# Kernel tuning notes

Measured on AMD Instinct MI355X. Metric: run time of the kernel, lower is better.

## Reference

```python
import jax, jax.numpy as jnp
import numpy as np
import math

DIM = 1024
MAX_DEPTH = 16
ROPE_BASE = 10000.0
NUM_ACTIVE = 2

def setup_inputs() -> dict:
    key = jax.random.key(0)
    ks = jax.random.split(key, 6)
    bsz, seq, dim, E, hidden = 4, 1024, DIM, 8, 4 * DIM
    bound = 1.0 / math.sqrt(dim)
    return {
        "x": jax.random.normal(ks[0], (bsz, seq, dim), jnp.float32),
        "router_w": jax.random.normal(ks[1], (dim, dim), jnp.float32) * 0.02,
        "expert_keys": jax.random.uniform(ks[2], (E, dim), jnp.float32, -bound, bound),
        "expert_bias": jnp.zeros((E,), jnp.float32),
        "fc_w": jax.random.normal(ks[3], (E, hidden, dim), jnp.float32) * 0.02,
        "proj_w": jax.random.normal(ks[4], (E, dim, hidden), jnp.float32) * 0.02,
        "depth_idx": 3,
    }

def _rope_row(depth_idx, rev_idx, dtype):
    half = DIM // 2
    inv_freq = 1.0 / (ROPE_BASE ** (jnp.arange(0, DIM, 2, dtype=jnp.float32) / DIM))  # [half]
    f = depth_idx * inv_freq
    r = rev_idx * inv_freq
    return (jnp.cos(f).astype(dtype), jnp.sin(f).astype(dtype),
            jnp.cos(r).astype(dtype), jnp.sin(r).astype(dtype))

def reference(x, router_w, expert_keys, expert_bias, fc_w, proj_w, depth_idx):
    bsz, seq, dim = x.shape
    N = bsz * seq
    flat_x = x.reshape(N, dim)
    # router + RMSNorm (no weight, eps = machine eps, matching F.rms_norm default)
    q = flat_x @ router_w.T
    eps = jnp.asarray(jnp.finfo(q.dtype).eps, q.dtype)
    q = q * jax.lax.rsqrt(jnp.mean(q * q, axis=-1, keepdims=True) + eps)
    # depth RoPE (forward freq on first half pairing, reverse freq on second half)
    half = dim // 2
    cos, sin, rcos, rsin = _rope_row(float(depth_idx), float(MAX_DEPTH - 1 - depth_idx), q.dtype)
    q1, q2 = q[..., :half], q[..., half:]
    q = jnp.concatenate((q1 * cos + q2 * sin, -q1 * rsin + q2 * rcos), axis=-1)
    # routing
    logits = (q @ expert_keys.T) / math.sqrt(dim)  # [N, E]
    gate_values = jax.nn.sigmoid(logits)
    biased = logits + expert_bias
    _, topk_idx = jax.lax.top_k(biased, NUM_ACTIVE)  # [N, k]
    topk_gates = jnp.take_along_axis(gate_values, topk_idx, axis=-1)
    topk_gates = topk_gates / jnp.clip(topk_gates.sum(-1, keepdims=True), 1e-9, None)
    gates = jnp.zeros_like(gate_values).at[jnp.arange(N)[:, None], topk_idx].set(topk_gates)
    # dense all-expert MLP: relu(x W_fc^T)^2 W_proj^T, then mask-and-sum
    h = jax.nn.relu(jnp.einsum('nd,ehd->neh', flat_x, fc_w))
    expert_out = jnp.einsum('neh,edh->ned', h * h, proj_w)  # [N, E, dim]
    y = jnp.einsum('ned,ne->nd', expert_out, gates)
    return y.reshape(bsz, seq, dim)
```

## Files before the change

kernel.cpp:

```cpp
#include <hip/hip_runtime.h>
#include <hip/hip_bf16.h>
#include <math.h>

#define N_TOK 4096
#define DIM_V 1024
#define NEXP  8
#define HID   4096
#define NSLOT 9216

typedef short  s16x8 __attribute__((ext_vector_type(8)));
typedef unsigned short u16x8 __attribute__((ext_vector_type(8)));
typedef float  f32x4 __attribute__((ext_vector_type(4)));

constexpr size_t OFF_XB   = 0;
constexpr size_t OFF_WB   = OFF_XB + 8388608;
constexpr size_t OFF_RK   = OFF_WB + 2097152;
constexpr size_t OFF_KPP  = OFF_RK + 65536;
constexpr size_t OFF_SSQ  = OFF_KPP + 65536;
constexpr size_t OFF_CNT  = OFF_SSQ + 16384;
constexpr size_t OFF_CUR  = OFF_CNT + 128;
constexpr size_t OFF_TOK  = OFF_CUR + 128;
constexpr size_t OFF_GSL  = OFF_TOK + 36864;
constexpr size_t ZERO_BEG = OFF_KPP;
constexpr size_t ZERO_END = OFF_GSL + 36864;
constexpr size_t OFF_OFFP = ZERO_END;
constexpr size_t OFF_IDX2 = OFF_OFFP + 128;
constexpr size_t OFF_G2   = OFF_IDX2 + 32768;
constexpr size_t OFF_INV  = OFF_G2 + 32768;
constexpr size_t SMALL_END = OFF_INV + 32768;

constexpr size_t A_OFF_FCB = SMALL_END;
constexpr size_t A_OFF_PO  = A_OFF_FCB;
constexpr size_t A_OFF_PJB = A_OFF_FCB + 67108864;
constexpr size_t A_OFF_H2  = A_OFF_PJB + 67108864;
constexpr size_t WS_FULL   = A_OFF_H2 + 75497472;

__device__ inline unsigned short f2bf(float f) {
  __hip_bfloat16 h = __float2bfloat16(f);
  return __builtin_bit_cast(unsigned short, h);
}

__device__ __forceinline__ void gload16(const void* g, void* l) {
  __builtin_amdgcn_global_load_lds(
      (const __attribute__((address_space(1))) unsigned int*)g,
      (__attribute__((address_space(3))) unsigned int*)l, 16, 0, 0);
}

__global__ void k_cvt(const float* __restrict__ s, unsigned short* __restrict__ d, int n8) {
  for (int i = blockIdx.x * blockDim.x + threadIdx.x; i < n8;
       i += gridDim.x * blockDim.x) {
    float4 a = ((const float4*)s)[2 * i];
    float4 b = ((const float4*)s)[2 * i + 1];
    u16x8 o = { f2bf(a.x), f2bf(a.y), f2bf(a.z), f2bf(a.w),
                f2bf(b.x), f2bf(b.y), f2bf(b.z), f2bf(b.w) };
    *(u16x8*)(d + (size_t)i * 8) = o;
  }
}

__global__ void k_ropekeys(const float* __restrict__ keys, const int* __restrict__ depth,
                           double* __restrict__ rk) {
  int i = threadIdx.x;
  if (i >= 512) return;
  int dep = depth[0];
  double p = pow(10000.0, (double)i / 512.0);
  float invf = 1.0f / (float)p;
  float ff = (float)dep * invf;
  float rr = (float)(15 - dep) * invf;
  float cf  = (float)cos((double)ff);
  float sf  = (float)sin((double)ff);
  float rcf = (float)cos((double)rr);
  float rsf = (float)sin((double)rr);
  for (int e = 0; e < NEXP; ++e) {
    double k1 = (double)keys[e * DIM_V + i];
    double k2 = (double)keys[e * DIM_V + 512 + i];
    rk[e * DIM_V + i]       = (double)cf  * k1 - (double)rsf * k2;
    rk[e * DIM_V + 512 + i] = (double)sf  * k1 + (double)rcf * k2;
  }
}

__global__ __launch_bounds__(256) void k_colsum(const float* __restrict__ W,
                                                const double* __restrict__ rk,
                                                double* __restrict__ kpp) {
  int j  = blockIdx.x * 256 + threadIdx.x;
  int d0 = blockIdx.y * 64;
  double acc[NEXP] = {};
  for (int dd = 0; dd < 64; ++dd) {
    int d = d0 + dd;
    double w = (double)W[(size_t)d * DIM_V + j];
#pragma unroll
    for (int e = 0; e < NEXP; ++e) acc[e] += w * rk[e * DIM_V + d];
  }
  for (int e = 0; e < NEXP; ++e) atomicAdd(&kpp[e * DIM_V + j], acc[e]);
}

__global__ __launch_bounds__(256) void k_qt(const unsigned short* __restrict__ xb,
                                            const unsigned short* __restrict__ wb,
                                            float* __restrict__ sumsq) {
  __shared__ alignas(16) unsigned short As[128][64];
  __shared__ alignas(16) unsigned short Bs[128][64];
  const int m0 = blockIdx.x * 128, n0 = blockIdx.y * 128;
  const int tid = threadIdx.x, wid = tid >> 6, lane = tid & 63;
  const int wr = (wid >> 1) * 64, wc = (wid & 1) * 64;
  const int srow = tid >> 3, scol = (tid & 7) * 8;
  f32x4 acc[4][4] = {};
  for (int k0 = 0; k0 < DIM_V; k0 += 64) {
    __syncthreads();
#pragma unroll
    for (int p = 0; p < 4; ++p)
      gload16(xb + (size_t)(m0 + p * 32 + srow) * DIM_V + k0 + scol,
              (char*)As + p * 4096 + wid * 1024);
#pragma unroll
    for (int p = 0; p < 4; ++p)
      gload16(wb + (size_t)(n0 + p * 32 + srow) * DIM_V + k0 + scol,
              (char*)Bs + p * 4096 + wid * 1024);
    __syncthreads();
#pragma unroll
    for (int kk = 0; kk < 64; kk += 32) {
      s16x8 af[4], bfv[4];
#pragma unroll
      for (int m = 0; m < 4; ++m)
        af[m] = *(const s16x8*)&As[wr + m * 16 + (lane & 15)][kk + (lane >> 4) * 8];
#pragma unroll
      for (int n = 0; n < 4; ++n)
        bfv[n] = *(const s16x8*)&Bs[wc + n * 16 + (lane & 15)][kk + (lane >> 4) * 8];
#pragma unroll
      for (int m = 0; m < 4; ++m)
#pragma unroll
        for (int n = 0; n < 4; ++n)
          acc[m][n] = __builtin_amdgcn_mfma_f32_16x16x32_bf16(af[m], bfv[n], acc[m][n], 0, 0, 0);
    }
  }
#pragma unroll
  for (int m = 0; m < 4; ++m)
#pragma unroll
    for (int j = 0; j < 4; ++j) {
      float s = 0.f;
#pragma unroll
      for (int n = 0; n < 4; ++n) { float v = acc[m][n][j]; s += v * v; }
      s += __shfl_xor(s, 1, 64); s += __shfl_xor(s, 2, 64);
      s += __shfl_xor(s, 4, 64); s += __shfl_xor(s, 8, 64);
      if ((lane & 15) == 0)
        atomicAdd(&sumsq[m0 + wr + m * 16 + (lane >> 4) * 4 + j], s);
    }
}

__global__ __launch_bounds__(256) void k_gate(const float* __restrict__ x,
                                              const double* __restrict__ kpp,
                                              const float* __restrict__ sumsq,
                                              const float* __restrict__ bias,
                                              int* __restrict__ idx2, float* __restrict__ gates2,
                                              int* __restrict__ counts) {
  int wave = (blockIdx.x * 256 + threadIdx.x) >> 6;
  int lane = threadIdx.x & 63;
  if (wave >= N_TOK) return;
  const float4* xr = (const float4*)(x + (size_t)wave * DIM_V);
  double a[NEXP] = {};
#pragma unroll
  for (int j = 0; j < 4; ++j) {
    int c = lane + 64 * j;
    float4 v = xr[c];
#pragma unroll
    for (int e = 0; e < NEXP; ++e) {
      const double* kp = kpp + (size_t)e * DIM_V + c * 4;
      a[e] += (double)v.x * kp[0] + (double)v.y * kp[1] +
              (double)v.z * kp[2] + (double)v.w * kp[3];
    }
  }
#pragma unroll
  for (int e = 0; e < NEXP; ++e)
    for (int d = 1; d < 64; d <<= 1) a[e] += __shfl_xor(a[e], d, 64);
  if (lane == 0) {
    float s = rsqrtf(sumsq[wave] * (1.0f / 1024.0f) + 1.1920928955078125e-7f);
    float z[NEXP], b[NEXP];
#pragma unroll
    for (int e = 0; e < NEXP; ++e) {
      z[e] = (float)(a[e] * (double)s * (1.0 / 32.0));
      b[e] = z[e] + bias[e];
    }
    int i1 = 0;
    for (int e = 1; e < NEXP; ++e) if (b[e] > b[i1]) i1 = e;
    int i2 = -1;
    for (int e = 0; e < NEXP; ++e) if (e != i1 && (i2 < 0 || b[e] > b[i2])) i2 = e;
    float g1 = 1.f / (1.f + expf(-z[i1]));
    float g2 = 1.f / (1.f + expf(-z[i2]));
    float sm = fmaxf(g1 + g2, 1e-9f);
    idx2[wave * 2] = i1; idx2[wave * 2 + 1] = i2;
    gates2[wave * 2] = g1 / sm; gates2[wave * 2 + 1] = g2 / sm;
    atomicAdd(&counts[i1], 1); atomicAdd(&counts[i2], 1);
  }
}

__global__ void k_prefix(const int* __restrict__ counts, int* __restrict__ offp) {
  if (threadIdx.x == 0) {
    int off = 0;
    for (int e = 0; e < NEXP; ++e) { offp[e] = off; off += (counts[e] + 127) & ~127; }
    offp[NEXP] = off;
  }
}

__global__ void k_scatter(const int* __restrict__ idx2, const float* __restrict__ gates2,
                          const int* __restrict__ offp, int* __restrict__ cursor,
                          int* __restrict__ tok, float* __restrict__ gsl,
                          int* __restrict__ inv) {
  int n = blockIdx.x * 256 + threadIdx.x;
  if (n >= N_TOK) return;
  for (int r = 0; r < 2; ++r) {
    int e = idx2[n * 2 + r];
    int pos = atomicAdd(&cursor[e], 1);
    int slot = offp[e] + pos;
    tok[slot] = n; gsl[slot] = gates2[n * 2 + r]; inv[n * 2 + r] = slot;
  }
}

template<int KD, int ONB, bool GATHER, bool FCEPI>
__global__ __launch_bounds__(256) void k_gemm(
    const unsigned short* __restrict__ Aptr,
    const unsigned short* __restrict__ Wptr,
    const int* __restrict__ offp, const int* __restrict__ tok,
    const float* __restrict__ gsl, void* __restrict__ outp) {
  constexpr int GNB = ONB / 128;
  constexpr int NT  = KD / 64;
  const int G = gridDim.x, q = G >> 3;
  const int idp = (blockIdx.x & 7) * q + (blockIdx.x >> 3);
  const int n0 = (idp % GNB) * 128, m0 = (idp / GNB) * 128;
  if (m0 >= offp[NEXP]) return;
  int e = 0; while (e < NEXP - 1 && m0 >= offp[e + 1]) ++e;
  const unsigned short* Bp = Wptr + ((size_t)e * ONB + n0) * KD;

  __shared__ alignas(16) char smem[65536];
  char* smb = smem;
  const int tid = threadIdx.x, wid = tid >> 6, lane = tid & 63;
  const int wr = (wid >> 1) * 64, wc = (wid & 1) * 64;
  const int rql  = tid >> 3;
  const int swc8 = ((tid & 7) ^ ((tid >> 3) & 7)) * 8;
  const int frow = lane & 15, fsl = lane >> 4, fsw = lane & 7;

  int arow[4];
#pragma unroll
  for (int p = 0; p < 4; ++p)
    arow[p] = GATHER ? tok[m0 + p * 32 + rql] : (m0 + p * 32 + rql);

  auto stage = [&](int k0s, unsigned db) {
#pragma unroll
    for (int p = 0; p < 4; ++p)
      gload16(Aptr + (size_t)arow[p] * KD + k0s + swc8,
              smb + db + p * 4096 + wid * 1024);
#pragma unroll
    for (int p = 0; p < 4; ++p)
      gload16(Bp + (size_t)(p * 32 + rql) * KD + k0s + swc8,
              smb + db + 16384 + p * 4096 + wid * 1024);
  };

  f32x4 acc[4][4] = {};
  stage(0, 0);
#pragma unroll 2
  for (int t = 0; t < NT; ++t) {
    int tn = t + 1; if (tn == NT) tn = 0;
    stage(tn * 64, (unsigned)((t + 1) & 1) * 32768u);
    asm volatile("s_waitcnt vmcnt(8)" ::: "memory");
    __builtin_amdgcn_s_barrier();
    __builtin_amdgcn_sched_barrier(0);
    const unsigned Ab = (unsigned)(t & 1) * 32768u, Bb = Ab + 16384u;
    s16x8 af[2][4], bfr[2][4];
#pragma unroll
    for (int kk2 = 0; kk2 < 2; ++kk2) {
      const unsigned so = (unsigned)(((fsl + kk2 * 4) ^ fsw) << 4);
#pragma unroll
      for (int m = 0; m < 4; ++m)
        af[kk2][m] = *(const s16x8*)(smb + Ab + (unsigned)(wr + m * 16 + frow) * 128 + so);
#pragma unroll
      for (int n = 0; n < 4; ++n)
        bfr[kk2][n] = *(const s16x8*)(smb + Bb + (unsigned)(wc + n * 16 + frow) * 128 + so);
    }
    __builtin_amdgcn_s_setprio(1);
#pragma unroll
    for (int kk2 = 0; kk2 < 2; ++kk2)
#pragma unroll
      for (int m = 0; m < 4; ++m)
#pragma unroll
        for (int n = 0; n < 4; ++n)
          acc[m][n] = __builtin_amdgcn_mfma_f32_16x16x32_bf16(af[kk2][m], bfr[kk2][n],
                                                              acc[m][n], 0, 0, 0);
    __builtin_amdgcn_s_setprio(0);
    __builtin_amdgcn_sched_barrier(0);
    __builtin_amdgcn_s_barrier();
  }

#pragma unroll
  for (int m = 0; m < 4; ++m)
#pragma unroll
    for (int j = 0; j < 4; ++j) {
      const int grow = m0 + wr + m * 16 + (lane >> 4) * 4 + j;
      if constexpr (FCEPI) {
        unsigned short* out = (unsigned short*)outp;
#pragma unroll
        for (int n = 0; n < 4; ++n) {
          float v = acc[m][n][j];
          v = v > 0.f ? v * v : 0.f;
          out[(size_t)grow * ONB + n0 + wc + n * 16 + (lane & 15)] = f2bf(v);
        }
      } else {
        float* out = (float*)outp;
        const float g = gsl[grow];
#pragma unroll
        for (int n = 0; n < 4; ++n)
          out[(size_t)grow * ONB + n0 + wc + n * 16 + (lane & 15)] = acc[m][n][j] * g;
      }
    }
}

__global__ void k_combine(const float* __restrict__ po, const int* __restrict__ inv,
                          float* __restrict__ y) {
  const int total = N_TOK * (DIM_V / 4);
  for (int i = blockIdx.x * blockDim.x + threadIdx.x; i < total;
       i += gridDim.x * blockDim.x) {
    int n = i >> 8, c = i & 255;
    int s1 = inv[n * 2], s2 = inv[n * 2 + 1];
    float4 a = ((const float4*)(po + (size_t)s1 * DIM_V))[c];
    float4 b = ((const float4*)(po + (size_t)s2 * DIM_V))[c];
    float4 o; o.x = a.x + b.x; o.y = a.y + b.y; o.z = a.z + b.z; o.w = a.w + b.w;
    ((float4*)(y + (size_t)n * DIM_V))[c] = o;
  }
}

extern "C" void kernel_launch(void* const* d_in, const int* in_sizes, int n_in,
                              void* d_out, int out_size, void* d_ws, size_t ws_size,
                              hipStream_t stream) {
  if (ws_size < WS_FULL) return;
  const float* x      = (const float*)d_in[0];
  const float* rw     = (const float*)d_in[1];
  const float* keys   = (const float*)d_in[2];
  const float* bias   = (const float*)d_in[3];
  const float* fc_w   = (const float*)d_in[4];
  const float* proj_w = (const float*)d_in[5];
  const int*   depth  = (const int*)d_in[6];
  char* ws = (char*)d_ws;
  unsigned short* xb  = (unsigned short*)(ws + OFF_XB);
  unsigned short* wb  = (unsigned short*)(ws + OFF_WB);
  double* rk    = (double*)(ws + OFF_RK);
  double* kpp   = (double*)(ws + OFF_KPP);
  float*  ssq   = (float*)(ws + OFF_SSQ);
  int*    cnt   = (int*)(ws + OFF_CNT);
  int*    cur   = (int*)(ws + OFF_CUR);
  int*    tok   = (int*)(ws + OFF_TOK);
  float*  gsl   = (float*)(ws + OFF_GSL);
  int*    offp  = (int*)(ws + OFF_OFFP);
  int*    idx2  = (int*)(ws + OFF_IDX2);
  float*  g2    = (float*)(ws + OFF_G2);
  int*    inv   = (int*)(ws + OFF_INV);
  unsigned short* fcb = (unsigned short*)(ws + A_OFF_FCB);
  unsigned short* pjb = (unsigned short*)(ws + A_OFF_PJB);
  unsigned short* h2  = (unsigned short*)(ws + A_OFF_H2);
  float*  po    = (float*)(ws + A_OFF_PO);
  float*  y     = (float*)d_out;

  hipMemsetAsync(ws + ZERO_BEG, 0, ZERO_END - ZERO_BEG, stream);
  k_cvt<<<1024, 256, 0, stream>>>(x,  xb, (N_TOK * DIM_V) / 8);
  k_cvt<<<512,  256, 0, stream>>>(rw, wb, (DIM_V * DIM_V) / 8);
  k_cvt<<<2048, 256, 0, stream>>>(fc_w,   fcb, (NEXP * HID * DIM_V) / 8);
  k_cvt<<<2048, 256, 0, stream>>>(proj_w, pjb, (NEXP * DIM_V * HID) / 8);
  k_ropekeys<<<1, 512, 0, stream>>>(keys, depth, rk);
  k_colsum<<<dim3(4, 16), 256, 0, stream>>>(rw, rk, kpp);
  k_qt<<<dim3(32, 8), 256, 0, stream>>>(xb, wb, ssq);
  k_gate<<<1024, 256, 0, stream>>>(x, kpp, ssq, bias, idx2, g2, cnt);
  k_prefix<<<1, 64, 0, stream>>>(cnt, offp);
  k_scatter<<<16, 256, 0, stream>>>(idx2, g2, offp, cur, tok, gsl, inv);
  k_gemm<DIM_V, HID,   true,  true ><<<dim3((NSLOT / 128) * (HID / 128)),   256, 0, stream>>>(
      xb, fcb, offp, tok, gsl, h2);
  k_gemm<HID,   DIM_V, false, false><<<dim3((NSLOT / 128) * (DIM_V / 128)), 256, 0, stream>>>(
      h2, pjb, offp, tok, gsl, po);
  k_combine<<<2048, 256, 0, stream>>>(po, inv, y);
}
```

Measured before the change: 486.3 us.

## Merge conversion kernels, fold prefix into scatter, add 256x256 FC GEMM

Four fp32-to-bf16 conversion launches become one kernel, and the prefix-sum kernel is folded into scatter, which cuts launch overhead. The router GEMM now reuses the pipelined k_gemm template with a sum-of-squares epilogue. The expert FC GEMM moves to a new 512-thread kernel with a 256x256 tile, which gives more operand reuse per LDS load but uses 128KB of LDS. Grids are resized to 44x16 and 72x8 blocks, which risks occupancy loss and padded work on partial 256-row tiles.

Result: faster. 473.8 us (-2.6%).

```diff
diff --git a/kernel.cpp b/kernel.cpp
--- a/kernel.cpp
+++ b/kernel.cpp
@@ -46,14 +46,25 @@
       (__attribute__((address_space(3))) unsigned int*)l, 16, 0, 0);
 }
 
-__global__ void k_cvt(const float* __restrict__ s, unsigned short* __restrict__ d, int n8) {
-  for (int i = blockIdx.x * blockDim.x + threadIdx.x; i < n8;
+__global__ void k_cvt_all(const float* __restrict__ x, const float* __restrict__ rw,
+                          const float* __restrict__ fw, const float* __restrict__ pw,
+                          unsigned short* __restrict__ xb, unsigned short* __restrict__ wb,
+                          unsigned short* __restrict__ fcb, unsigned short* __restrict__ pjb) {
+  const int NX = (N_TOK * DIM_V) / 8, NW = (DIM_V * DIM_V) / 8;
+  const int NF = (NEXP * HID * DIM_V) / 8;
+  const int total = NX + NW + NF + NF;
+  for (int i = blockIdx.x * blockDim.x + threadIdx.x; i < total;
        i += gridDim.x * blockDim.x) {
-    float4 a = ((const float4*)s)[2 * i];
-    float4 b = ((const float4*)s)[2 * i + 1];
+    const float* s; unsigned short* d; int j;
+    if (i < NX)                { s = x;  d = xb;  j = i; }
+    else if (i < NX + NW)      { s = rw; d = wb;  j = i - NX; }
+    else if (i < NX + NW + NF) { s = fw; d = fcb; j = i - NX - NW; }
+    else                       { s = pw; d = pjb; j = i - NX - NW - NF; }
+    float4 a = ((const float4*)s)[2 * j];
+    float4 b = ((const float4*)s)[2 * j + 1];
     u16x8 o = { f2bf(a.x), f2bf(a.y), f2bf(a.z), f2bf(a.w),
                 f2bf(b.x), f2bf(b.y), f2bf(b.z), f2bf(b.w) };
-    *(u16x8*)(d + (size_t)i * 8) = o;
+    *(u16x8*)(d + (size_t)j * 8) = o;
   }
 }
 
@@ -93,57 +104,6 @@
   for (int e = 0; e < NEXP; ++e) atomicAdd(&kpp[e * DIM_V + j], acc[e]);
 }
 
-__global__ __launch_bounds__(256) void k_qt(const unsigned short* __restrict__ xb,
-                                            const unsigned short* __restrict__ wb,
-                                            float* __restrict__ sumsq) {
-  __shared__ alignas(16) unsigned short As[128][64];
-  __shared__ alignas(16) unsigned short Bs[128][64];
-  const int m0 = blockIdx.x * 128, n0 = blockIdx.y * 128;
-  const int tid = threadIdx.x, wid = tid >> 6, lane = tid & 63;
-  const int wr = (wid >> 1) * 64, wc = (wid & 1) * 64;
-  const int srow = tid >> 3, scol = (tid & 7) * 8;
-  f32x4 acc[4][4] = {};
-  for (int k0 = 0; k0 < DIM_V; k0 += 64) {
-    __syncthreads();
-#pragma unroll
-    for (int p = 0; p < 4; ++p)
-      gload16(xb + (size_t)(m0 + p * 32 + srow) * DIM_V + k0 + scol,
-              (char*)As + p * 4096 + wid * 1024);
-#pragma unroll
-    for (int p = 0; p < 4; ++p)
-      gload16(wb + (size_t)(n0 + p * 32 + srow) * DIM_V + k0 + scol,
-              (char*)Bs + p * 4096 + wid * 1024);
-    __syncthreads();
-#pragma unroll
-    for (int kk = 0; kk < 64; kk += 32) {
-      s16x8 af[4], bfv[4];
-#pragma unroll
-      for (int m = 0; m < 4; ++m)
-        af[m] = *(const s16x8*)&As[wr + m * 16 + (lane & 15)][kk + (lane >> 4) * 8];
-#pragma unroll
-      for (int n = 0; n < 4; ++n)
-        bfv[n] = *(const s16x8*)&Bs[wc + n * 16 + (lane & 15)][kk + (lane >> 4) * 8];
-#pragma unroll
-      for (int m = 0; m < 4; ++m)
-#pragma unroll
-        for (int n = 0; n < 4; ++n)
-          acc[m][n] = __builtin_amdgcn_mfma_f32_16x16x32_bf16(af[m], bfv[n], acc[m][n], 0, 0, 0);
-    }
-  }
-#pragma unroll
-  for (int m = 0; m < 4; ++m)
-#pragma unroll
-    for (int j = 0; j < 4; ++j) {
-      float s = 0.f;
-#pragma unroll
-      for (int n = 0; n < 4; ++n) { float v = acc[m][n][j]; s += v * v; }
-      s += __shfl_xor(s, 1, 64); s += __shfl_xor(s, 2, 64);
-      s += __shfl_xor(s, 4, 64); s += __shfl_xor(s, 8, 64);
-      if ((lane & 15) == 0)
-        atomicAdd(&sumsq[m0 + wr + m * 16 + (lane >> 4) * 4 + j], s);
-    }
-}
-
 __global__ __launch_bounds__(256) void k_gate(const float* __restrict__ x,
                                               const double* __restrict__ kpp,
                                               const float* __restrict__ sumsq,
@@ -190,65 +150,150 @@
   }
 }
 
-__global__ void k_prefix(const int* __restrict__ counts, int* __restrict__ offp) {
-  if (threadIdx.x == 0) {
-    int off = 0;
-    for (int e = 0; e < NEXP; ++e) { offp[e] = off; off += (counts[e] + 127) & ~127; }
-    offp[NEXP] = off;
-  }
-}
-
 __global__ void k_scatter(const int* __restrict__ idx2, const float* __restrict__ gates2,
-                          const int* __restrict__ offp, int* __restrict__ cursor,
+                          const int* __restrict__ counts, int* __restrict__ cursor,
                           int* __restrict__ tok, float* __restrict__ gsl,
-                          int* __restrict__ inv) {
+                          int* __restrict__ inv, int* __restrict__ offp_out) {
+  int off[NEXP + 1];
+  off[0] = 0;
+  for (int e = 0; e < NEXP; ++e) off[e + 1] = off[e] + ((counts[e] + 127) & ~127);
   int n = blockIdx.x * 256 + threadIdx.x;
+  if (blockIdx.x == 0 && threadIdx.x == 0)
+    for (int e = 0; e <= NEXP; ++e) offp_out[e] = off[e];
   if (n >= N_TOK) return;
   for (int r = 0; r < 2; ++r) {
     int e = idx2[n * 2 + r];
     int pos = atomicAdd(&cursor[e], 1);
-    int slot = offp[e] + pos;
+    int slot = off[e] + pos;
     tok[slot] = n; gsl[slot] = gates2[n * 2 + r]; inv[n * 2 + r] = slot;
   }
 }
 
-template<int KD, int ONB, bool GATHER, bool FCEPI>
+__global__ __launch_bounds__(512) void k_fc256(
+    const unsigned short* __restrict__ xb,
+    const unsigned short* __restrict__ fcb,
+    const int* __restrict__ offp, const int* __restrict__ tok,
+    unsigned short* __restrict__ h2) {
+  constexpr int KD = DIM_V;
+  constexpr int NT = KD / 64;
+  const int G = gridDim.x, q = G >> 3;
+  const int idp = ((int)blockIdx.x & 7) * q + ((int)blockIdx.x >> 3);
+  const int bx = idp >> 4;
+  const int n0 = (idp & 15) * 256;
+  int c = 0, e = 0, m0 = -1;
+  for (e = 0; e < NEXP; ++e) {
+    int nb = (offp[e + 1] - offp[e] + 255) >> 8;
+    if (bx < c + nb) { m0 = offp[e] + (bx - c) * 256; break; }
+    c += nb;
+  }
+  if (m0 < 0) return;
+  const int segend = offp[e + 1];
+  const unsigned short* Bp = fcb + ((size_t)e * HID + n0) * KD;
+
+  __shared__ alignas(16) char smem[131072];
+  const int tid = threadIdx.x, wid = tid >> 6, lane = tid & 63;
+  const int wr = (wid >> 2) * 128, wcc = (wid & 3) * 64;
+  const int swc8 = ((tid & 7) ^ ((tid >> 3) & 7)) * 8;
+  const int frow = lane & 15, fsl = lane >> 4, fkey = lane & 7;
+
+  int arow[4];
+#pragma unroll
+  for (int p = 0; p < 4; ++p) {
+    int rr = m0 + p * 64 + (tid >> 3);
+    arow[p] = tok[rr < NSLOT ? rr : NSLOT - 1];
+  }
+
+  auto stage = [&](int k0s, unsigned db) {
+#pragma unroll
+    for (int p = 0; p < 4; ++p)
+      gload16(xb + (size_t)arow[p] * KD + k0s + swc8,
+              smem + db + p * 8192 + wid * 1024);
+#pragma unroll
+    for (int p = 0; p < 4; ++p)
+      gload16(Bp + (size_t)(p * 64 + (tid >> 3)) * KD + k0s + swc8,
+              smem + db + 32768 + p * 8192 + wid * 1024);
+  };
+
+  f32x4 acc[8][4] = {};
+  stage(0, 0);
+  for (int t = 0; t < NT; ++t) {
+    int tn = t + 1; if (tn == NT) tn = 0;
+    stage(tn * 64, (unsigned)((t + 1) & 1) * 65536u);
+    asm volatile("s_waitcnt vmcnt(8)" ::: "memory");
+    __builtin_amdgcn_s_barrier();
+    __builtin_amdgcn_sched_barrier(0);
+    const unsigned Ab = (unsigned)(t & 1) * 65536u, Bb = Ab + 32768u;
+#pragma unroll
+    for (int kk2 = 0; kk2 < 2; ++kk2) {
+      const unsigned so = (unsigned)(((fsl + kk2 * 4) ^ fkey) << 4);
+      s16x8 af[8], bfr[4];
+#pragma unroll
+      for (int m = 0; m < 8; ++m)
+        af[m] = *(const s16x8*)(smem + Ab + (unsigned)(wr + m * 16 + frow) * 128 + so);
+#pragma unroll
+      for (int n = 0; n < 4; ++n)
+        bfr[n] = *(const s16x8*)(smem + Bb + (unsigned)(wcc + n * 16 + frow) * 128 + so);
+      __builtin_amdgcn_s_setprio(1);
+#pragma unroll
+      for (int m = 0; m < 8; ++m)
+#pragma unroll
+        for (int n = 0; n < 4; ++n)
+          acc[m][n] = __builtin_amdgcn_mfma_f32_16x16x32_bf16(af[m], bfr[n], acc[m][n], 0, 0, 0);
+      __builtin_amdgcn_s_setprio(0);
+    }
+    __builtin_amdgcn_sched_barrier(0);
+    __builtin_amdgcn_s_barrier();
+  }
+#pragma unroll
+  for (int m = 0; m < 8; ++m)
+#pragma unroll
+    for (int j = 0; j < 4; ++j) {
+      const int grow = m0 + wr + m * 16 + (lane >> 4) * 4 + j;
+      if (grow < segend) {
+#pragma unroll
+        for (int n = 0; n < 4; ++n) {
+          float v = acc[m][n][j];
+          v = v > 0.f ? v * v : 0.f;
+          h2[(size_t)grow * HID + n0 + wcc + n * 16 + (lane & 15)] = f2bf(v);
+        }
+      }
+    }
+}
+
+template<int KD, int ONB, int EPI>
 __global__ __launch_bounds__(256) void k_gemm(
     const unsigned short* __restrict__ Aptr,
     const unsigned short* __restrict__ Wptr,
-    const int* __restrict__ offp, const int* __restrict__ tok,
+    const int* __restrict__ offp,
     const float* __restrict__ gsl, void* __restrict__ outp) {
   constexpr int GNB = ONB / 128;
   constexpr int NT  = KD / 64;
   const int G = gridDim.x, q = G >> 3;
-  const int idp = (blockIdx.x & 7) * q + (blockIdx.x >> 3);
+  const int idp = ((int)blockIdx.x & 7) * q + ((int)blockIdx.x >> 3);
   const int n0 = (idp % GNB) * 128, m0 = (idp / GNB) * 128;
-  if (m0 >= offp[NEXP]) return;
-  int e = 0; while (e < NEXP - 1 && m0 >= offp[e + 1]) ++e;
+  int e = 0;
+  if constexpr (EPI == 1) {
+    if (m0 >= offp[NEXP]) return;
+    while (e < NEXP - 1 && m0 >= offp[e + 1]) ++e;
+  }
   const unsigned short* Bp = Wptr + ((size_t)e * ONB + n0) * KD;
 
   __shared__ alignas(16) char smem[65536];
-  char* smb = smem;
   const int tid = threadIdx.x, wid = tid >> 6, lane = tid & 63;
   const int wr = (wid >> 1) * 64, wc = (wid & 1) * 64;
   const int rql  = tid >> 3;
   const int swc8 = ((tid & 7) ^ ((tid >> 3) & 7)) * 8;
-  const int frow = lane & 15, fsl = lane >> 4, fsw = lane & 7;
-
-  int arow[4];
-#pragma unroll
-  for (int p = 0; p < 4; ++p)
-    arow[p] = GATHER ? tok[m0 + p * 32 + rql] : (m0 + p * 32 + rql);
+  const int frow = lane & 15, fsl = lane >> 4, fkey = lane & 7;
 
   auto stage = [&](int k0s, unsigned db) {
 #pragma unroll
     for (int p = 0; p < 4; ++p)
-      gload16(Aptr + (size_t)arow[p] * KD + k0s + swc8,
-              smb + db + p * 4096 + wid * 1024);
+      gload16(Aptr + (size_t)(m0 + p * 32 + rql) * KD + k0s + swc8,
+              smem + db + p * 4096 + wid * 1024);
 #pragma unroll
     for (int p = 0; p < 4; ++p)
       gload16(Bp + (size_t)(p * 32 + rql) * KD + k0s + swc8,
-              smb + db + 16384 + p * 4096 + wid * 1024);
+              smem + db + 16384 + p * 4096 + wid * 1024);
   };
 
   f32x4 acc[4][4] = {};
@@ -264,13 +309,13 @@
     s16x8 af[2][4], bfr[2][4];
 #pragma unroll
     for (int kk2 = 0; kk2 < 2; ++kk2) {
-      const unsigned so = (unsigned)(((fsl + kk2 * 4) ^ fsw) << 4);
+      const unsigned so = (unsigned)(((fsl + kk2 * 4) ^ fkey) << 4);
 #pragma unroll
       for (int m = 0; m < 4; ++m)
-        af[kk2][m] = *(const s16x8*)(smb + Ab + (unsigned)(wr + m * 16 + frow) * 128 + so);
+        af[kk2][m] = *(const s16x8*)(smem + Ab + (unsigned)(wr + m * 16 + frow) * 128 + so);
 #pragma unroll
       for (int n = 0; n < 4; ++n)
-        bfr[kk2][n] = *(const s16x8*)(smb + Bb + (unsigned)(wc + n * 16 + frow) * 128 + so);
+        bfr[kk2][n] = *(const s16x8*)(smem + Bb + (unsigned)(wc + n * 16 + frow) * 128 + so);
     }
     __builtin_amdgcn_s_setprio(1);
 #pragma unroll
@@ -291,14 +336,13 @@
 #pragma unroll
     for (int j = 0; j < 4; ++j) {
       const int grow = m0 + wr + m * 16 + (lane >> 4) * 4 + j;
-      if constexpr (FCEPI) {
-        unsigned short* out = (unsigned short*)outp;
-#pragma unroll
-        for (int n = 0; n < 4; ++n) {
-          float v = acc[m][n][j];
-          v = v > 0.f ? v * v : 0.f;
-          out[(size_t)grow * ONB + n0 + wc + n * 16 + (lane & 15)] = f2bf(v);
-        }
+      if constexpr (EPI == 0) {
+        float s = 0.f;
+#pragma unroll
+        for (int n = 0; n < 4; ++n) { float v = acc[m][n][j]; s += v * v; }
+        s += __shfl_xor(s, 1, 64); s += __shfl_xor(s, 2, 64);
+        s += __shfl_xor(s, 4, 64); s += __shfl_xor(s, 8, 64);
+        if ((lane & 15) == 0) atomicAdd(&((float*)outp)[grow], s);
       } else {
         float* out = (float*)outp;
         const float g = gsl[grow];
@@ -355,19 +399,13 @@
   float*  y     = (float*)d_out;
 
   hipMemsetAsync(ws + ZERO_BEG, 0, ZERO_END - ZERO_BEG, stream);
-  k_cvt<<<1024, 256, 0, stream>>>(x,  xb, (N_TOK * DIM_V) / 8);
-  k_cvt<<<512,  256, 0, stream>>>(rw, wb, (DIM_V * DIM_V) / 8);
-  k_cvt<<<2048, 256, 0, stream>>>(fc_w,   fcb, (NEXP * HID * DIM_V) / 8);
-  k_cvt<<<2048, 256, 0, stream>>>(proj_w, pjb, (NEXP * DIM_V * HID) / 8);
+  k_cvt_all<<<2048, 256, 0, stream>>>(x, rw, fc_w, proj_w, xb, wb, fcb, pjb);
   k_ropekeys<<<1, 512, 0, stream>>>(keys, depth, rk);
   k_colsum<<<dim3(4, 16), 256, 0, stream>>>(rw, rk, kpp);
-  k_qt<<<dim3(32, 8), 256, 0, stream>>>(xb, wb, ssq);
+  k_gemm<DIM_V, DIM_V, 0><<<dim3(32 * 8), 256, 0, stream>>>(xb, wb, offp, gsl, ssq);
   k_gate<<<1024, 256, 0, stream>>>(x, kpp, ssq, bias, idx2, g2, cnt);
-  k_prefix<<<1, 64, 0, stream>>>(cnt, offp);
-  k_scatter<<<16, 256, 0, stream>>>(idx2, g2, offp, cur, tok, gsl, inv);
-  k_gemm<DIM_V, HID,   true,  true ><<<dim3((NSLOT / 128) * (HID / 128)),   256, 0, stream>>>(
-      xb, fcb, offp, tok, gsl, h2);
-  k_gemm<HID,   DIM_V, false, false><<<dim3((NSLOT / 128) * (DIM_V / 128)), 256, 0, stream>>>(
-      h2, pjb, offp, tok, gsl, po);
+  k_scatter<<<16, 256, 0, stream>>>(idx2, g2, cnt, cur, tok, gsl, inv, offp);
+  k_fc256<<<dim3(44 * 16), 512, 0, stream>>>(xb, fcb, offp, tok, h2);
+  k_gemm<HID, DIM_V, 1><<<dim3(72 * 8), 256, 0, stream>>>(h2, pjb, offp, gsl, po);
   k_combine<<<2048, 256, 0, stream>>>(po, inv, y);
 }
```
